# Performance work log

Hardware: AMD Instinct MI355X
Metric: run time of the kernel (lower is better)

The kernel has to match this reference:

```python
import jax, jax.numpy as jnp
import numpy as np

B, T, M, P = 512, 64, 256, 256


def setup_inputs() -> dict:
    key = jax.random.key(0)
    ks = jax.random.split(key, 17)
    w = lambda i, shape: (jax.random.normal(ks[i], shape, jnp.float32) * 0.05)
    return {
        "encoded_inputs": jax.random.normal(ks[0], (B, T, M), jnp.float32),
        "y": jax.random.normal(ks[1], (B, T, 1), jnp.float32),
        "tar": jax.random.normal(ks[2], (B, 2), jnp.float32),
        "train": 1,
        "Wd_w": w(3, (M, 2 * P)), "Wd_b": w(4, (M,)),
        "Ud_w": w(5, (M, M)),
        "vd_w": w(6, (1, M)),
        "wt_w": w(7, (1, M + 1)), "wt_b": w(8, (1,)),
        "Wy_w": w(9, (P, P + M)), "Wy_b": w(10, (P,)),
        "vy_w": w(11, (1, P)), "vy_b": w(12, (1,)),
        "Wih": w(13, (4 * P, 1)), "Whh": w(14, (4 * P, P)),
        "bih": w(15, (4 * P,)), "bhh": w(16, (4 * P,)),
    }


def _lstm_cell(x, h, c, Wih, Whh, bih, bhh):
    # torch.nn.LSTMCell gate order: i, f, g, o
    g = x @ Wih.T + h @ Whh.T + (bih + bhh)
    i, f, gg, o = jnp.split(g, 4, axis=1)
    c = jax.nn.sigmoid(f) * c + jax.nn.sigmoid(i) * jnp.tanh(gg)
    h = jax.nn.sigmoid(o) * jnp.tanh(c)
    return h, c


def reference(encoded_inputs, y, tar, train,
              Wd_w, Wd_b, Ud_w, vd_w, wt_w, wt_b,
              Wy_w, Wy_b, vy_w, vy_b, Wih, Whh, bih, bhh):
    Bn = encoded_inputs.shape[0]
    Pn = Whh.shape[1]
    Mn = encoded_inputs.shape[2]
    h0 = jnp.zeros((Bn, Pn), encoded_inputs.dtype)
    c0 = jnp.zeros((Bn, Pn), encoded_inputs.dtype)
    ctx0 = jnp.zeros((Bn, Mn), encoded_inputs.dtype)
    # U_d(encoded_inputs) is loop-invariant
    y1 = jnp.einsum('btm,nm->btn', encoded_inputs, Ud_w)  # (B,T,M)

    def attend(h, s):
        x1 = jnp.concatenate([h, s], axis=1) @ Wd_w.T + Wd_b      # (B,M)
        z1 = jnp.tanh(x1[:, None, :] + y1)                        # (B,T,M)
        l = jnp.einsum('btm,m->bt', z1, vd_w[0])                  # (B,T)
        beta = jax.nn.softmax(l, axis=1)
        return jnp.einsum('bt,btm->bm', beta, encoded_inputs)     # (B,M)

    def step(carry, y_t):
        h, s, _ = carry
        c_t = attend(h, s)
        y_til = jnp.concatenate([c_t, y_t], axis=1) @ wt_w.T + wt_b  # (B,1)
        h, s = _lstm_cell(y_til, h, s, Wih, Whh, bih, bhh)
        return (h, s, c_t), None

    (h, s, c_t), _ = jax.lax.scan(step, (h0, c0, ctx0), jnp.swapaxes(y, 0, 1))

    def head(h):
        return (jnp.concatenate([h, c_t], axis=1) @ Wy_w.T + Wy_b) @ vy_w.T + vy_b

    def extra(h, s, inp):
        y_til = jnp.concatenate([c_t, inp], axis=1) @ wt_w.T + wt_b
        h, s = _lstm_cell(y_til, h, s, Wih, Whh, bih, bhh)
        return h, s, head(h)

    y_Tp1 = head(h)
    if train:
        h, s, y_Tp2 = extra(h, s, tar[:, 0:1])
        h, s, y_Tp3 = extra(h, s, tar[:, 1:2])
    else:
        h, s, y_Tp2 = extra(h, s, y_Tp1)
        h, s, y_Tp3 = extra(h, s, y_Tp2)
    return (y_Tp1, y_Tp2, y_Tp3)
```

## Files before the change

kernel.cpp:

```cpp
#include <hip/hip_runtime.h>


typedef unsigned short u16;
typedef unsigned int u32;
typedef _Float16 half_t;
typedef half_t h2 __attribute__((ext_vector_type(2)));

#define BB 512
#define TT 64
#define MM 256
#define PP 256
#define YS 264
#define ES 68
#define NROW 2
#define NTH 1024

#define WD16_OFF  0
#define WHH16_OFF 131072
#define WY16_OFF  393216
#define WQ_ELEMS  524288
#define WQ_BYTES  (WQ_ELEMS * 2)

struct H8 { h2 p[4]; };

#if defined(__has_builtin)
#if __has_builtin(__builtin_amdgcn_fdot2)
#define FDOT2(a, b, c) __builtin_amdgcn_fdot2((a), (b), (c), false)
#endif
#endif
#ifndef FDOT2
__device__ __forceinline__ float FDOT2(h2 a, h2 b, float c) {
  return c + (float)a[0] * (float)b[0] + (float)a[1] * (float)b[1];
}
#endif

__device__ __forceinline__ float dot8(const H8 w, const H8 a, float acc) {
  acc = FDOT2(w.p[0], a.p[0], acc);
  acc = FDOT2(w.p[1], a.p[1], acc);
  acc = FDOT2(w.p[2], a.p[2], acc);
  acc = FDOT2(w.p[3], a.p[3], acc);
  return acc;
}
__device__ __forceinline__ u16 f2h(float f) {
  union { half_t h; u16 u; } x; x.h = (half_t)f; return x.u;
}
__device__ __forceinline__ float h2f(u16 u) {
  union { u16 u; half_t h; } x; x.u = u; return (float)x.h;
}
__device__ __forceinline__ void unpackH8(const H8 v, float f[8]) {
#pragma unroll
  for (int i = 0; i < 8; ++i) f[i] = (float)v.p[i >> 1][i & 1];
}
__device__ __forceinline__ void ldf8(const float* p, float f[8]) {
  float4 a = *(const float4*)p;
  float4 b = *(const float4*)(p + 4);
  f[0]=a.x; f[1]=a.y; f[2]=a.z; f[3]=a.w;
  f[4]=b.x; f[5]=b.y; f[6]=b.z; f[7]=b.w;
}
__device__ __forceinline__ float tanh_fast(float x) {
  float e = __builtin_amdgcn_exp2f(x * 2.885390081777927f);
  return 1.0f - 2.0f * __builtin_amdgcn_rcpf(1.0f + e);
}
__device__ __forceinline__ float sigmoid_fast(float x) {
  float e = __builtin_amdgcn_exp2f(x * -1.4426950408889634f);
  return __builtin_amdgcn_rcpf(1.0f + e);
}

__global__ __launch_bounds__(256) void prep_kernel(
    const float* __restrict__ Wd, const float* __restrict__ Whh,
    const float* __restrict__ Wy, u16* __restrict__ o) {
  int i = blockIdx.x * 256 + threadIdx.x;
  float v;
  if (i < WHH16_OFF) {
    int ki = i & 7, n = (i >> 3) & 255, kb = i >> 11;
    v = Wd[n * 512 + kb * 8 + ki];
  } else if (i < WY16_OFF) {
    int r = i - WHH16_OFF;
    int ki = r & 7, n = (r >> 3) & 1023, kb = r >> 13;
    v = Whh[n * 256 + kb * 8 + ki];
  } else {
    int r = i - WY16_OFF;
    int ki = r & 7, n = (r >> 3) & 255, kb = r >> 11;
    v = Wy[n * 512 + kb * 8 + ki];
  }
  o[i] = f2h(v);
}

template <int WQ>
__global__ __launch_bounds__(NTH, 4) void scan_kernel(
    const float* __restrict__ E,
    const float* __restrict__ yin,
    const float* __restrict__ tar,
    const int*   __restrict__ train,
    const void*  __restrict__ Wd_q,
    const float* __restrict__ Wd_b,
    const float* __restrict__ Ud_w,
    const float* __restrict__ vd_w,
    const float* __restrict__ wt_w,
    const float* __restrict__ wt_b,
    const void*  __restrict__ Wy_q,
    const float* __restrict__ Wy_b,
    const float* __restrict__ vy_w,
    const float* __restrict__ vy_b,
    const float* __restrict__ Wih,
    const void*  __restrict__ Whh_q,
    const float* __restrict__ bih,
    const float* __restrict__ bhh,
    float* __restrict__ out)
{
  __shared__ __align__(16) u16   y1l[NROW][TT * YS];
  __shared__ __align__(16) u16   e16T[NROW][MM * ES];
  __shared__ __align__(16) u32   hs16[NROW][256];
  __shared__ __align__(16) u32   ctx16p[NROW][128];
  __shared__ __align__(16) float px1[4][MM];
  __shared__ __align__(16) float pg[6][MM];
  __shared__ __align__(16) float pg3[4][MM];
  __shared__ __align__(16) float lpart[NROW][8][TT];
  __shared__ __align__(16) u16   betas16[NROW][TT];
  __shared__ __align__(16) float ysh[NROW][TT];
  __shared__ float red[16];
  __shared__ float sc[NROW];

  const int j   = threadIdx.x;
  const int n   = j & 255;
  const int grp = j >> 8;
  const int wv  = j >> 6;
  const int b0  = blockIdx.x * NROW;

  if (j < 512) ((u32*)hs16)[j] = 0;
  float creg0 = 0.f, creg1 = 0.f;

  const float wih0 = Wih[n],       wih1 = Wih[n + 256];
  const float wih2 = Wih[n + 512], wih3 = Wih[n + 768];
  const float bb0 = bih[n]       + bhh[n];
  const float bb1 = bih[n + 256] + bhh[n + 256];
  const float bb2 = bih[n + 512] + bhh[n + 512];
  const float bb3 = bih[n + 768] + bhh[n + 768];
  const float wtM = wt_w[MM], wtb = wt_b[0];

  if (j < NROW * TT)
    ysh[j >> 6][j & 63] = yin[(size_t)(b0 + (j >> 6)) * TT + (j & 63)];

  {
    const float* __restrict__ Eb0 = E + (size_t)b0 * TT * MM;
    for (int i = j; i < NROW * TT * MM; i += NTH) {
      int r = i >> 14;
      int idx = i & 16383;
      int t = idx >> 8, m = idx & 255;
      e16T[r][m * ES + t] = f2h(Eb0[i]);
    }
  }

  {
    const int rs = grp >> 1, ths = grp & 1;
    const float* __restrict__ Eb = E + (size_t)(b0 + rs) * TT * MM;
    const float* __restrict__ Uj = Ud_w + (size_t)n * MM;
    for (int t0 = ths * 32; t0 < ths * 32 + 32; t0 += 16) {
      float acc[16];
#pragma unroll
      for (int i = 0; i < 16; ++i) acc[i] = 0.f;
      for (int m0 = 0; m0 < MM; m0 += 8) {
        float w[8]; ldf8(Uj + m0, w);
#pragma unroll
        for (int tt = 0; tt < 16; ++tt) {
          float e[8]; ldf8(Eb + (size_t)(t0 + tt) * MM + m0, e);
#pragma unroll
          for (int mm = 0; mm < 8; ++mm) acc[tt] = fmaf(e[mm], w[mm], acc[tt]);
        }
      }
#pragma unroll
      for (int tt = 0; tt < 16; ++tt)
        y1l[rs][(t0 + tt) * YS + n] = f2h(acc[tt]);
    }
  }
  __syncthreads();

  auto gates_apply = [&](int r, float gi, float gf, float gg, float go,
                         float ytil) {
    gi += ytil * wih0 + bb0;
    gf += ytil * wih1 + bb1;
    gg += ytil * wih2 + bb2;
    go += ytil * wih3 + bb3;
    float& cr = r ? creg1 : creg0;
    float c = sigmoid_fast(gf) * cr + sigmoid_fast(gi) * tanh_fast(gg);
    float h = sigmoid_fast(go) * tanh_fast(c);
    cr = c;
    u16* hsu = (u16*)hs16[r];
    hsu[n] = f2h(h);
    hsu[256 + n] = f2h(c);
  };

  auto head_store = [&](int outIdx) {
    float p = 0.f;
    const int rr = grp >> 1, seg = grp & 1;
    const u32* st = seg ? ctx16p[rr] : hs16[rr];
    if (WQ) {
      const u16* pw = (const u16*)Wy_q + ((size_t)(seg * 32) * 256 + n) * 8;
#pragma unroll 2
      for (int kb = 0; kb < 32; ++kb) {
        H8 w = *(const H8*)pw; pw += 2048;
        H8 s = *(const H8*)&st[kb * 4];
        p = dot8(w, s, p);
      }
    } else {
      const float* W = (const float*)Wy_q + (size_t)n * 512 + seg * 256;
#pragma unroll 2
      for (int kb = 0; kb < 32; ++kb) {
        H8 sv = *(const H8*)&st[kb * 4];
        float sf[8]; unpackH8(sv, sf);
        float w[8]; ldf8(W + kb * 8, w);
#pragma unroll
        for (int i = 0; i < 8; ++i) p = fmaf(sf[i], w[i], p);
      }
    }
    if (grp) px1[grp - 1][n] = p;
    __syncthreads();
    if (grp == 0) {
      float q0 = (p + px1[0][n] + Wy_b[n]) * vy_w[n];
      float q1 = (px1[1][n] + px1[2][n] + Wy_b[n]) * vy_w[n];
#pragma unroll
      for (int off = 32; off; off >>= 1) {
        q0 += __shfl_xor(q0, off, 64);
        q1 += __shfl_xor(q1, off, 64);
      }
      if ((j & 63) == 0) { red[wv] = q0; red[8 + wv] = q1; }
    }
    __syncthreads();
    if (j == 0) {
      float o0 = red[0] + red[1] + red[2] + red[3] + vy_b[0];
      float o1 = red[8] + red[9] + red[10] + red[11] + vy_b[0];
      out[(size_t)outIdx * BB + b0] = o0;
      out[(size_t)outIdx * BB + b0 + 1] = o1;
      sc[0] = o0; sc[1] = o1;
    }
    __syncthreads();
  };

  auto mv4 = [&](float& m0, float& m1, float& m2, float& m3, float& m4,
                 float& m5) {
    m0 = m1 = m2 = m3 = m4 = m5 = 0.f;
    if (WQ) {
      const u16* Whh16 = (const u16*)Whh_q;
      if (grp < 2) {
        const int kb0 = grp << 4;
        const u16* pw = Whh16 + ((size_t)kb0 * 1024 + n) * 8;
#pragma unroll 2
        for (int kb2 = 0; kb2 < 16; ++kb2) {
          const int kb = kb0 + kb2;
          H8 h0 = *(const H8*)&hs16[0][kb * 4];
          H8 h1 = *(const H8*)&hs16[1][kb * 4];
          H8 w0 = *(const H8*)pw;
          H8 w1 = *(const H8*)(pw + 2048);
          H8 w2 = *(const H8*)(pw + 4096);
          pw += 8192;
          m0 = dot8(w0, h0, m0); m1 = dot8(w0, h1, m1);
          m2 = dot8(w1, h0, m2); m3 = dot8(w1, h1, m3);
          m4 = dot8(w2, h0, m4); m5 = dot8(w2, h1, m5);
        }
      } else {
        const int half = grp - 2;
        const u16* p3 = Whh16 + ((size_t)(half * 16) * 1024 + 768 + n) * 8;
#pragma unroll 2
        for (int kb2 = 0; kb2 < 16; ++kb2) {
          const int kg = half * 16 + kb2;
          H8 w3 = *(const H8*)p3; p3 += 8192;
          H8 h0 = *(const H8*)&hs16[0][kg * 4];
          H8 h1 = *(const H8*)&hs16[1][kg * 4];
          m0 = dot8(w3, h0, m0); m1 = dot8(w3, h1, m1);
        }
      }
    } else {
      const float* Whf = (const float*)Whh_q;
      if (grp < 2) {
        const int kb0 = grp << 4;
        const float* pw0 = Whf + (size_t)n * 256 + kb0 * 8;
        const float* pw1 = pw0 + 256 * 256;
        const float* pw2 = pw0 + 512 * 256;
#pragma unroll 2
        for (int kb2 = 0; kb2 < 16; ++kb2) {
          const int kb = kb0 + kb2;
          H8 h0v = *(const H8*)&hs16[0][kb * 4];
          H8 h1v = *(const H8*)&hs16[1][kb * 4];
          float hf0[8], hf1[8]; unpackH8(h0v, hf0); unpackH8(h1v, hf1);
          float w0[8], w1[8], w2[8];
          ldf8(pw0 + kb2 * 8, w0);
          ldf8(pw1 + kb2 * 8, w1);
          ldf8(pw2 + kb2 * 8, w2);
#pragma unroll
          for (int i = 0; i < 8; ++i) {
            m0 = fmaf(hf0[i], w0[i], m0); m1 = fmaf(hf1[i], w0[i], m1);
            m2 = fmaf(hf0[i], w1[i], m2); m3 = fmaf(hf1[i], w1[i], m3);
            m4 = fmaf(hf0[i], w2[i], m4); m5 = fmaf(hf1[i], w2[i], m5);
          }
        }
      } else {
        const int half = grp - 2;
        const float* p3f = Whf + ((size_t)(768 + n)) * 256 + half * 128;
#pragma unroll 2
        for (int kb2 = 0; kb2 < 16; ++kb2) {
          const int kg = half * 16 + kb2;
          H8 h0v = *(const H8*)&hs16[0][kg * 4];
          H8 h1v = *(const H8*)&hs16[1][kg * 4];
          float hf0[8], hf1[8]; unpackH8(h0v, hf0); unpackH8(h1v, hf1);
          float w3[8]; ldf8(p3f + kb2 * 8, w3);
#pragma unroll
          for (int i = 0; i < 8; ++i) {
            m0 = fmaf(hf0[i], w3[i], m0); m1 = fmaf(hf1[i], w3[i], m1);
          }
        }
      }
    }
  };

  for (int step = 0; step < TT; ++step) {
    float s0 = 0.f, s1 = 0.f, s2 = 0.f, s3 = 0.f, s4 = 0.f, s5 = 0.f;
    {
      float a0 = 0, a1 = 0, a2 = 0, a3 = 0, a4 = 0, a5 = 0;
      if (WQ) {
        const u16* Whh16 = (const u16*)Whh_q;
        if (grp < 2) {
          const int kb0 = grp << 4;
          const u16* pw = Whh16 + ((size_t)kb0 * 1024 + n) * 8;
#pragma unroll 2
          for (int kb2 = 0; kb2 < 16; ++kb2) {
            const int kb = kb0 + kb2;
            H8 h0 = *(const H8*)&hs16[0][kb * 4];
            H8 h1 = *(const H8*)&hs16[1][kb * 4];
            H8 w0 = *(const H8*)pw;
            H8 w1 = *(const H8*)(pw + 2048);
            H8 w2 = *(const H8*)(pw + 4096);
            pw += 8192;
            a0 = dot8(w0, h0, a0); a1 = dot8(w0, h1, a1);
            a2 = dot8(w1, h0, a2); a3 = dot8(w1, h1, a3);
            a4 = dot8(w2, h0, a4); a5 = dot8(w2, h1, a5);
          }
        } else {
          const int half = grp - 2;
          const u16* pd = (const u16*)Wd_q + ((size_t)(half * 32) * 256 + n) * 8;
          const u16* p3 = Whh16 + ((size_t)(half * 16) * 1024 + 768 + n) * 8;
#pragma unroll 2
          for (int kb2 = 0; kb2 < 16; ++kb2) {
            const int kd = half * 32 + kb2 * 2;
            const int kg = half * 16 + kb2;
            H8 s00 = *(const H8*)&hs16[0][kd * 4];
            H8 s01 = *(const H8*)&hs16[0][kd * 4 + 4];
            H8 s10 = *(const H8*)&hs16[1][kd * 4];
            H8 s11 = *(const H8*)&hs16[1][kd * 4 + 4];
            H8 wd0 = *(const H8*)pd;
            H8 wd1 = *(const H8*)(pd + 2048);
            pd += 4096;
            H8 w3 = *(const H8*)p3; p3 += 8192;
            H8 h0 = *(const H8*)&hs16[0][kg * 4];
            H8 h1 = *(const H8*)&hs16[1][kg * 4];
            a0 = dot8(wd0, s00, a0); a0 = dot8(wd1, s01, a0);
            a1 = dot8(wd0, s10, a1); a1 = dot8(wd1, s11, a1);
            a2 = dot8(w3, h0, a2);   a3 = dot8(w3, h1, a3);
          }
        }
      } else {
        const float* Whf = (const float*)Whh_q;
        if (grp < 2) {
          const int kb0 = grp << 4;
          const float* pw0 = Whf + (size_t)n * 256 + kb0 * 8;
          const float* pw1 = pw0 + 256 * 256;
          const float* pw2 = pw0 + 512 * 256;
#pragma unroll 2
          for (int kb2 = 0; kb2 < 16; ++kb2) {
            const int kb = kb0 + kb2;
            H8 h0v = *(const H8*)&hs16[0][kb * 4];
            H8 h1v = *(const H8*)&hs16[1][kb * 4];
            float hf0[8], hf1[8]; unpackH8(h0v, hf0); unpackH8(h1v, hf1);
            float w0[8], w1[8], w2[8];
            ldf8(pw0 + kb2 * 8, w0);
            ldf8(pw1 + kb2 * 8, w1);
            ldf8(pw2 + kb2 * 8, w2);
#pragma unroll
            for (int i = 0; i < 8; ++i) {
              a0 = fmaf(hf0[i], w0[i], a0); a1 = fmaf(hf1[i], w0[i], a1);
              a2 = fmaf(hf0[i], w1[i], a2); a3 = fmaf(hf1[i], w1[i], a3);
              a4 = fmaf(hf0[i], w2[i], a4); a5 = fmaf(hf1[i], w2[i], a5);
            }
          }
        } else {
          const int half = grp - 2;
          const float* Wdf = (const float*)Wd_q + (size_t)n * 512 + half * 256;
          const float* p3f = Whf + ((size_t)(768 + n)) * 256 + half * 128;
#pragma unroll 2
          for (int kb2 = 0; kb2 < 16; ++kb2) {
            const int kd = half * 32 + kb2 * 2;
            const int kg = half * 16 + kb2;
            H8 s00v = *(const H8*)&hs16[0][kd * 4];
            H8 s01v = *(const H8*)&hs16[0][kd * 4 + 4];
            H8 s10v = *(const H8*)&hs16[1][kd * 4];
            H8 s11v = *(const H8*)&hs16[1][kd * 4 + 4];
            float f00[8], f01[8], f10[8], f11[8];
            unpackH8(s00v, f00); unpackH8(s01v, f01);
            unpackH8(s10v, f10); unpackH8(s11v, f11);
            H8 h0v = *(const H8*)&hs16[0][kg * 4];
            H8 h1v = *(const H8*)&hs16[1][kg * 4];
            float hf0[8], hf1[8]; unpackH8(h0v, hf0); unpackH8(h1v, hf1);
            float wd0[8], wd1[8], w3[8];
            ldf8(Wdf + kb2 * 16, wd0);
            ldf8(Wdf + kb2 * 16 + 8, wd1);
            ldf8(p3f + kb2 * 8, w3);
#pragma unroll
            for (int i = 0; i < 8; ++i) {
              a0 = fmaf(f00[i], wd0[i], a0); a0 = fmaf(f01[i], wd1[i], a0);
              a1 = fmaf(f10[i], wd0[i], a1); a1 = fmaf(f11[i], wd1[i], a1);
              a2 = fmaf(hf0[i], w3[i], a2);  a3 = fmaf(hf1[i], w3[i], a3);
            }
          }
        }
      }
      if (grp == 0) {
        s0 = a0; s1 = a1; s2 = a2; s3 = a3; s4 = a4; s5 = a5;
      } else if (grp == 1) {
        pg[0][n] = a0; pg[1][n] = a1; pg[2][n] = a2;
        pg[3][n] = a3; pg[4][n] = a4; pg[5][n] = a5;
      } else if (grp == 2) {
        float bia = Wd_b[n];
        px1[0][n] = a0 + bia; px1[1][n] = a1 + bia;
        pg3[0][n] = a2; pg3[1][n] = a3;
      } else {
        px1[2][n] = a0; px1[3][n] = a1;
        pg3[2][n] = a2; pg3[3][n] = a3;
      }
    }
    __syncthreads();

    {
      const int r = j >> 9, e8 = (j >> 6) & 7, t = j & 63;
      const u16* __restrict__ yrow = &y1l[r][t * YS + e8 * 32];
      const float* __restrict__ xh = &px1[r][e8 * 32];
      const float* __restrict__ xc = &px1[2 + r][e8 * 32];
      const float* __restrict__ vp = vd_w + e8 * 32;
      float lp = 0.f;
#pragma unroll
      for (int m0 = 0; m0 < 32; m0 += 8) {
        H8 yv = *(const H8*)(yrow + m0);
        float yf[8]; unpackH8(yv, yf);
        float xf[8]; ldf8(xh + m0, xf);
        float xg[8]; ldf8(xc + m0, xg);
        float vf[8]; ldf8(vp + m0, vf);
#pragma unroll
        for (int mm = 0; mm < 8; ++mm) {
          float z = tanh_fast(xf[mm] + xg[mm] + yf[mm]);
          lp = fmaf(z, vf[mm], lp);
        }
      }
      lpart[r][e8][t] = lp;
    }
    __syncthreads();

    if ((j & 511) < 64) {
      const int r = j >> 9, t = j & 63;
      float l = lpart[r][0][t] + lpart[r][1][t] + lpart[r][2][t] +
                lpart[r][3][t] + lpart[r][4][t] + lpart[r][5][t] +
                lpart[r][6][t] + lpart[r][7][t];
      float mx = l;
#pragma unroll
      for (int off = 32; off; off >>= 1) mx = fmaxf(mx, __shfl_xor(mx, off, 64));
      float e = __builtin_amdgcn_exp2f((l - mx) * 1.4426950408889634f);
      float sm = e;
#pragma unroll
      for (int off = 32; off; off >>= 1) sm += __shfl_xor(sm, off, 64);
      betas16[r][t] = f2h(e * __builtin_amdgcn_rcpf(sm));
    }
    __syncthreads();

    if (((j >> 8) & 1) == 0) {
      const int r = j >> 9;
      const u16* __restrict__ ep = &e16T[r][n * ES];
      float acc = 0.f;
#pragma unroll
      for (int t0 = 0; t0 < TT; t0 += 8) {
        h2 e0 = *(const h2*)(ep + t0);
        h2 e1 = *(const h2*)(ep + t0 + 2);
        h2 e2 = *(const h2*)(ep + t0 + 4);
        h2 e3 = *(const h2*)(ep + t0 + 6);
        H8 bp = *(const H8*)&betas16[r][t0];
        acc = FDOT2(bp.p[0], e0, acc);
        acc = FDOT2(bp.p[1], e1, acc);
        acc = FDOT2(bp.p[2], e2, acc);
        acc = FDOT2(bp.p[3], e3, acc);
      }
      ((u16*)ctx16p[r])[n] = f2h(acc);
      float p = acc * wt_w[n];
#pragma unroll
      for (int off = 32; off; off >>= 1) p += __shfl_xor(p, off, 64);
      if ((j & 63) == 0) red[wv] = p;
    }
    __syncthreads();

    if (grp == 0) {
      float yt0 = red[0] + red[1] + red[2] + red[3] + ysh[0][step] * wtM + wtb;
      float yt1 = red[8] + red[9] + red[10] + red[11] + ysh[1][step] * wtM + wtb;
      gates_apply(0, s0 + pg[0][n], s2 + pg[2][n], s4 + pg[4][n],
                  pg3[0][n] + pg3[2][n], yt0);
      gates_apply(1, s1 + pg[1][n], s3 + pg[3][n], s5 + pg[5][n],
                  pg3[1][n] + pg3[3][n], yt1);
    }
    __syncthreads();
  }

  if (((j >> 8) & 1) == 0) {
    const int r = j >> 9;
    float p = h2f(((const u16*)ctx16p[r])[n]) * wt_w[n];
#pragma unroll
    for (int off = 32; off; off >>= 1) p += __shfl_xor(p, off, 64);
    if ((j & 63) == 0) red[wv] = p;
  }
  __syncthreads();
  const float ctd0 = red[0] + red[1] + red[2] + red[3];
  const float ctd1 = red[8] + red[9] + red[10] + red[11];

  head_store(0);

  const int tr = train[0];
  for (int e = 0; e < 2; ++e) {
    float m0, m1, m2, m3, m4, m5;
    mv4(m0, m1, m2, m3, m4, m5);
    if (grp == 1) {
      pg[0][n] = m0; pg[1][n] = m1; pg[2][n] = m2;
      pg[3][n] = m3; pg[4][n] = m4; pg[5][n] = m5;
    } else if (grp == 2) {
      pg3[0][n] = m0; pg3[1][n] = m1;
    } else if (grp == 3) {
      pg3[2][n] = m0; pg3[3][n] = m1;
    }
    __syncthreads();
    if (grp == 0) {
      float inp0 = tr ? tar[(size_t)b0 * 2 + e] : sc[0];
      float inp1 = tr ? tar[(size_t)(b0 + 1) * 2 + e] : sc[1];
      float yt0 = ctd0 + inp0 * wtM + wtb;
      float yt1 = ctd1 + inp1 * wtM + wtb;
      gates_apply(0, m0 + pg[0][n], m2 + pg[2][n], m4 + pg[4][n],
                  pg3[0][n] + pg3[2][n], yt0);
      gates_apply(1, m1 + pg[1][n], m3 + pg[3][n], m5 + pg[5][n],
                  pg3[1][n] + pg3[3][n], yt1);
    }
    __syncthreads();
    head_store(1 + e);
  }
}

extern "C" void kernel_launch(void* const* d_in, const int* in_sizes, int n_in,
                              void* d_out, int out_size, void* d_ws, size_t ws_size,
                              hipStream_t stream) {
  const float* E     = (const float*)d_in[0];
  const float* yin   = (const float*)d_in[1];
  const float* tar   = (const float*)d_in[2];
  const int*   train = (const int*)d_in[3];
  const float* Wd_w  = (const float*)d_in[4];
  const float* Wd_b  = (const float*)d_in[5];
  const float* Ud_w  = (const float*)d_in[6];
  const float* vd_w  = (const float*)d_in[7];
  const float* wt_w  = (const float*)d_in[8];
  const float* wt_b  = (const float*)d_in[9];
  const float* Wy_w  = (const float*)d_in[10];
  const float* Wy_b  = (const float*)d_in[11];
  const float* vy_w  = (const float*)d_in[12];
  const float* vy_b  = (const float*)d_in[13];
  const float* Wih   = (const float*)d_in[14];
  const float* Whh   = (const float*)d_in[15];
  const float* bih   = (const float*)d_in[16];
  const float* bhh   = (const float*)d_in[17];

  float* out = (float*)d_out;

  if (ws_size >= (size_t)WQ_BYTES) {
    u16* wq = (u16*)d_ws;
    prep_kernel<<<dim3(WQ_ELEMS / 256), dim3(256), 0, stream>>>(
        Wd_w, Whh, Wy_w, wq);
    scan_kernel<1><<<dim3(BB / NROW), dim3(NTH), 0, stream>>>(
        E, yin, tar, train, wq + WD16_OFF, Wd_b, Ud_w, vd_w, wt_w, wt_b,
        wq + WY16_OFF, Wy_b, vy_w, vy_b, Wih, wq + WHH16_OFF, bih, bhh, out);
  } else {
    scan_kernel<0><<<dim3(BB / NROW), dim3(NTH), 0, stream>>>(
        E, yin, tar, train, Wd_w, Wd_b, Ud_w, vd_w, wt_w, wt_b,
        Wy_w, Wy_b, vy_w, vy_b, Wih, Whh, bih, bhh, out);
  }

  (void)in_sizes; (void)n_in; (void)out_size;
}
```

Before: 1.087 ms.

## Fuse softmax into context pass per wave and software-pipeline rotated weight loads

Each of the 8 waves in the first 512 threads now recomputes the softmax for its batch row and writes a private beta copy. This removes one block-wide barrier between the softmax and the context dot product, and threads are remapped to rows by j>>8 with the red[] layout adjusted to match. The recurrent matvec loops are also double-buffered by hand, and the k-block start is rotated per block group to spread global/L2 access across blocks. The cost is redundant exp/shuffle work and more registers for the prefetched weights.

```diff
diff --git a/kernel.cpp b/kernel.cpp
--- a/kernel.cpp
+++ b/kernel.cpp
@@ -9,7 +9,6 @@
 #define BB 512
 #define TT 64
 #define MM 256
-#define PP 256
 #define YS 264
 #define ES 68
 #define NROW 2
@@ -116,7 +115,7 @@
   __shared__ __align__(16) float pg[6][MM];
   __shared__ __align__(16) float pg3[4][MM];
   __shared__ __align__(16) float lpart[NROW][8][TT];
-  __shared__ __align__(16) u16   betas16[NROW][TT];
+  __shared__ __align__(16) u16   betas16[8][TT];
   __shared__ __align__(16) float ysh[NROW][TT];
   __shared__ float red[16];
   __shared__ float sc[NROW];
@@ -126,6 +125,7 @@
   const int grp = j >> 8;
   const int wv  = j >> 6;
   const int b0  = blockIdx.x * NROW;
+  const int rot = (blockIdx.x >> 3) & 15;
 
   if (j < 512) ((u32*)hs16)[j] = 0;
   float creg0 = 0.f, creg1 = 0.f;
@@ -223,12 +223,12 @@
         q0 += __shfl_xor(q0, off, 64);
         q1 += __shfl_xor(q1, off, 64);
       }
-      if ((j & 63) == 0) { red[wv] = q0; red[8 + wv] = q1; }
+      if ((j & 63) == 0) { red[wv] = q0; red[4 + wv] = q1; }
     }
     __syncthreads();
     if (j == 0) {
       float o0 = red[0] + red[1] + red[2] + red[3] + vy_b[0];
-      float o1 = red[8] + red[9] + red[10] + red[11] + vy_b[0];
+      float o1 = red[4] + red[5] + red[6] + red[7] + vy_b[0];
       out[(size_t)outIdx * BB + b0] = o0;
       out[(size_t)outIdx * BB + b0 + 1] = o1;
       sc[0] = o0; sc[1] = o1;
@@ -320,41 +320,104 @@
         const u16* Whh16 = (const u16*)Whh_q;
         if (grp < 2) {
           const int kb0 = grp << 4;
-          const u16* pw = Whh16 + ((size_t)kb0 * 1024 + n) * 8;
-#pragma unroll 2
-          for (int kb2 = 0; kb2 < 16; ++kb2) {
-            const int kb = kb0 + kb2;
-            H8 h0 = *(const H8*)&hs16[0][kb * 4];
-            H8 h1 = *(const H8*)&hs16[1][kb * 4];
-            H8 w0 = *(const H8*)pw;
-            H8 w1 = *(const H8*)(pw + 2048);
-            H8 w2 = *(const H8*)(pw + 4096);
-            pw += 8192;
-            a0 = dot8(w0, h0, a0); a1 = dot8(w0, h1, a1);
-            a2 = dot8(w1, h0, a2); a3 = dot8(w1, h1, a3);
-            a4 = dot8(w2, h0, a4); a5 = dot8(w2, h1, a5);
+          const u16* __restrict__ wb = Whh16 + ((size_t)kb0 * 1024 + n) * 8;
+          H8 wa0, wa1, wa2, wb0, wb1, wb2;
+          {
+            const u16* p = wb + (size_t)rot * 8192;
+            wa0 = *(const H8*)p;
+            wa1 = *(const H8*)(p + 2048);
+            wa2 = *(const H8*)(p + 4096);
+          }
+#pragma unroll
+          for (int kb2 = 0; kb2 < 16; kb2 += 2) {
+            {
+              const int kr = (kb2 + 1 + rot) & 15;
+              const u16* p = wb + (size_t)kr * 8192;
+              wb0 = *(const H8*)p;
+              wb1 = *(const H8*)(p + 2048);
+              wb2 = *(const H8*)(p + 4096);
+            }
+            {
+              const int kb = kb0 + ((kb2 + rot) & 15);
+              H8 h0 = *(const H8*)&hs16[0][kb * 4];
+              H8 h1 = *(const H8*)&hs16[1][kb * 4];
+              a0 = dot8(wa0, h0, a0); a1 = dot8(wa0, h1, a1);
+              a2 = dot8(wa1, h0, a2); a3 = dot8(wa1, h1, a3);
+              a4 = dot8(wa2, h0, a4); a5 = dot8(wa2, h1, a5);
+            }
+            if (kb2 < 14) {
+              const int kr = (kb2 + 2 + rot) & 15;
+              const u16* p = wb + (size_t)kr * 8192;
+              wa0 = *(const H8*)p;
+              wa1 = *(const H8*)(p + 2048);
+              wa2 = *(const H8*)(p + 4096);
+            }
+            {
+              const int kb = kb0 + ((kb2 + 1 + rot) & 15);
+              H8 h0 = *(const H8*)&hs16[0][kb * 4];
+              H8 h1 = *(const H8*)&hs16[1][kb * 4];
+              a0 = dot8(wb0, h0, a0); a1 = dot8(wb0, h1, a1);
+              a2 = dot8(wb1, h0, a2); a3 = dot8(wb1, h1, a3);
+              a4 = dot8(wb2, h0, a4); a5 = dot8(wb2, h1, a5);
+            }
           }
         } else {
           const int half = grp - 2;
-          const u16* pd = (const u16*)Wd_q + ((size_t)(half * 32) * 256 + n) * 8;
-          const u16* p3 = Whh16 + ((size_t)(half * 16) * 1024 + 768 + n) * 8;
-#pragma unroll 2
-          for (int kb2 = 0; kb2 < 16; ++kb2) {
-            const int kd = half * 32 + kb2 * 2;
-            const int kg = half * 16 + kb2;
-            H8 s00 = *(const H8*)&hs16[0][kd * 4];
-            H8 s01 = *(const H8*)&hs16[0][kd * 4 + 4];
-            H8 s10 = *(const H8*)&hs16[1][kd * 4];
-            H8 s11 = *(const H8*)&hs16[1][kd * 4 + 4];
-            H8 wd0 = *(const H8*)pd;
-            H8 wd1 = *(const H8*)(pd + 2048);
-            pd += 4096;
-            H8 w3 = *(const H8*)p3; p3 += 8192;
-            H8 h0 = *(const H8*)&hs16[0][kg * 4];
-            H8 h1 = *(const H8*)&hs16[1][kg * 4];
-            a0 = dot8(wd0, s00, a0); a0 = dot8(wd1, s01, a0);
-            a1 = dot8(wd0, s10, a1); a1 = dot8(wd1, s11, a1);
-            a2 = dot8(w3, h0, a2);   a3 = dot8(w3, h1, a3);
+          const u16* __restrict__ pdb =
+              (const u16*)Wd_q + ((size_t)(half * 32) * 256 + n) * 8;
+          const u16* __restrict__ p3b =
+              Whh16 + ((size_t)(half * 16) * 1024 + 768 + n) * 8;
+          H8 da0, da1, da2, db0, db1, db2;
+          {
+            const u16* pd = pdb + (size_t)rot * 4096;
+            da0 = *(const H8*)pd;
+            da1 = *(const H8*)(pd + 2048);
+            da2 = *(const H8*)(p3b + (size_t)rot * 8192);
+          }
+#pragma unroll
+          for (int kb2 = 0; kb2 < 16; kb2 += 2) {
+            {
+              const int kr = (kb2 + 1 + rot) & 15;
+              const u16* pd = pdb + (size_t)kr * 4096;
+              db0 = *(const H8*)pd;
+              db1 = *(const H8*)(pd + 2048);
+              db2 = *(const H8*)(p3b + (size_t)kr * 8192);
+            }
+            {
+              const int kr = (kb2 + rot) & 15;
+              const int kd = half * 32 + kr * 2;
+              const int kg = half * 16 + kr;
+              H8 s00 = *(const H8*)&hs16[0][kd * 4];
+              H8 s01 = *(const H8*)&hs16[0][kd * 4 + 4];
+              H8 s10 = *(const H8*)&hs16[1][kd * 4];
+              H8 s11 = *(const H8*)&hs16[1][kd * 4 + 4];
+              H8 h0 = *(const H8*)&hs16[0][kg * 4];
+              H8 h1 = *(const H8*)&hs16[1][kg * 4];
+              a0 = dot8(da0, s00, a0); a0 = dot8(da1, s01, a0);
+              a1 = dot8(da0, s10, a1); a1 = dot8(da1, s11, a1);
+              a2 = dot8(da2, h0, a2);  a3 = dot8(da2, h1, a3);
+            }
+            if (kb2 < 14) {
+              const int kr = (kb2 + 2 + rot) & 15;
+              const u16* pd = pdb + (size_t)kr * 4096;
+              da0 = *(const H8*)pd;
+              da1 = *(const H8*)(pd + 2048);
+              da2 = *(const H8*)(p3b + (size_t)kr * 8192);
+            }
+            {
+              const int kr = (kb2 + 1 + rot) & 15;
+              const int kd = half * 32 + kr * 2;
+              const int kg = half * 16 + kr;
+              H8 s00 = *(const H8*)&hs16[0][kd * 4];
+              H8 s01 = *(const H8*)&hs16[0][kd * 4 + 4];
+              H8 s10 = *(const H8*)&hs16[1][kd * 4];
+              H8 s11 = *(const H8*)&hs16[1][kd * 4 + 4];
+              H8 h0 = *(const H8*)&hs16[0][kg * 4];
+              H8 h1 = *(const H8*)&hs16[1][kg * 4];
+              a0 = dot8(db0, s00, a0); a0 = dot8(db1, s01, a0);
+              a1 = dot8(db0, s10, a1); a1 = dot8(db1, s11, a1);
+              a2 = dot8(db2, h0, a2);  a3 = dot8(db2, h1, a3);
+            }
           }
         }
       } else {
@@ -452,11 +515,11 @@
     }
     __syncthreads();
 
-    if ((j & 511) < 64) {
-      const int r = j >> 9, t = j & 63;
-      float l = lpart[r][0][t] + lpart[r][1][t] + lpart[r][2][t] +
-                lpart[r][3][t] + lpart[r][4][t] + lpart[r][5][t] +
-                lpart[r][6][t] + lpart[r][7][t];
+    if (j < 512) {
+      const int r = j >> 8, lane = j & 63;
+      float l = lpart[r][0][lane] + lpart[r][1][lane] + lpart[r][2][lane] +
+                lpart[r][3][lane] + lpart[r][4][lane] + lpart[r][5][lane] +
+                lpart[r][6][lane] + lpart[r][7][lane];
       float mx = l;
 #pragma unroll
       for (int off = 32; off; off >>= 1) mx = fmaxf(mx, __shfl_xor(mx, off, 64));
@@ -464,25 +527,22 @@
       float sm = e;
 #pragma unroll
       for (int off = 32; off; off >>= 1) sm += __shfl_xor(sm, off, 64);
-      betas16[r][t] = f2h(e * __builtin_amdgcn_rcpf(sm));
-    }
-    __syncthreads();
-
-    if (((j >> 8) & 1) == 0) {
-      const int r = j >> 9;
+      betas16[wv][lane] = f2h(e * __builtin_amdgcn_rcpf(sm));
+      asm volatile("s_waitcnt lgkmcnt(0)" ::: "memory");
+      const u16* __restrict__ bp = betas16[wv];
       const u16* __restrict__ ep = &e16T[r][n * ES];
       float acc = 0.f;
 #pragma unroll
       for (int t0 = 0; t0 < TT; t0 += 8) {
+        H8 bv = *(const H8*)(bp + t0);
         h2 e0 = *(const h2*)(ep + t0);
         h2 e1 = *(const h2*)(ep + t0 + 2);
         h2 e2 = *(const h2*)(ep + t0 + 4);
         h2 e3 = *(const h2*)(ep + t0 + 6);
-        H8 bp = *(const H8*)&betas16[r][t0];
-        acc = FDOT2(bp.p[0], e0, acc);
-        acc = FDOT2(bp.p[1], e1, acc);
-        acc = FDOT2(bp.p[2], e2, acc);
-        acc = FDOT2(bp.p[3], e3, acc);
+        acc = FDOT2(bv.p[0], e0, acc);
+        acc = FDOT2(bv.p[1], e1, acc);
+        acc = FDOT2(bv.p[2], e2, acc);
+        acc = FDOT2(bv.p[3], e3, acc);
       }
       ((u16*)ctx16p[r])[n] = f2h(acc);
       float p = acc * wt_w[n];
@@ -494,7 +554,7 @@
 
     if (grp == 0) {
       float yt0 = red[0] + red[1] + red[2] + red[3] + ysh[0][step] * wtM + wtb;
-      float yt1 = red[8] + red[9] + red[10] + red[11] + ysh[1][step] * wtM + wtb;
+      float yt1 = red[4] + red[5] + red[6] + red[7] + ysh[1][step] * wtM + wtb;
       gates_apply(0, s0 + pg[0][n], s2 + pg[2][n], s4 + pg[4][n],
                   pg3[0][n] + pg3[2][n], yt0);
       gates_apply(1, s1 + pg[1][n], s3 + pg[3][n], s5 + pg[5][n],
@@ -503,8 +563,8 @@
     __syncthreads();
   }
 
-  if (((j >> 8) & 1) == 0) {
-    const int r = j >> 9;
+  if (j < 512) {
+    const int r = j >> 8;
     float p = h2f(((const u16*)ctx16p[r])[n]) * wt_w[n];
 #pragma unroll
     for (int off = 32; off; off >>= 1) p += __shfl_xor(p, off, 64);
@@ -512,7 +572,7 @@
   }
   __syncthreads();
   const float ctd0 = red[0] + red[1] + red[2] + red[3];
-  const float ctd1 = red[8] + red[9] + red[10] + red[11];
+  const float ctd1 = red[4] + red[5] + red[6] + red[7];
 
   head_store(0);
 
```

Measured after the change: 2.810 ms. 2.58x slower.
